# Kernel tuning notes

Hardware: AMD Instinct MI355X
Metric: run time of the kernel (lower is better)

## Reference

```python
import jax, jax.numpy as jnp
import numpy as np


def setup_inputs() -> dict:
    key = jax.random.key(0)
    k1, k2 = jax.random.split(key)
    D, N, M = 256, 1024, 1024
    z_x = jax.random.normal(k1, (1, D, N), dtype=jnp.float32)
    z_y = jax.random.normal(k2, (1, D, M), dtype=jnp.float32)
    return {"z_x": z_x, "z_y": z_y}


def reference(z_x, z_y):
    # squeeze().t(): (1, d, N) -> (N, d)
    x = jnp.squeeze(z_x).T  # (N, d)
    y = jnp.squeeze(z_y).T  # (M, d)
    # L1 compare: s[i, j] = -sum_d |x[i, d] - y[j, d]|  -> (N, M)
    s = -jnp.sum(jnp.abs(x[:, None, :] - y[None, :, :]), axis=-1)
    a = jax.nn.softmax(s, axis=1)  # row-wise softmax
    b = jax.nn.softmax(s, axis=0)  # column-wise softmax
    a = a + b - a * b              # soft union of alignments
    return jnp.sum(a * s) / jnp.sum(a)
```

## Files before the change

kernel.cpp:

```cpp
#include <hip/hip_runtime.h>
#include <math.h>


#define DD 256
#define NN 1024
#define DS 4
#define CH (DD / DS)
#define NQ (NN / 4)

__device__ __forceinline__ float waveMax(float v) {
  #pragma unroll
  for (int off = 32; off; off >>= 1) v = fmaxf(v, __shfl_xor(v, off, 64));
  return v;
}
__device__ __forceinline__ float waveSum(float v) {
  #pragma unroll
  for (int off = 32; off; off >>= 1) v += __shfl_xor(v, off, 64);
  return v;
}
__device__ __forceinline__ float blockMax(float v, float* red) {
  v = waveMax(v);
  __syncthreads();
  if ((threadIdx.x & 63) == 0) red[threadIdx.x >> 6] = v;
  __syncthreads();
  return fmaxf(fmaxf(red[0], red[1]), fmaxf(red[2], red[3]));
}
__device__ __forceinline__ float blockSum(float v, float* red) {
  v = waveSum(v);
  __syncthreads();
  if ((threadIdx.x & 63) == 0) red[threadIdx.x >> 6] = v;
  __syncthreads();
  return red[0] + red[1] + red[2] + red[3];
}


#define SSTEP(YB, dd)                                                          \
  {                                                                            \
    const float* xp_ = xs + (dd) * 32 + g * 8;                                 \
    const float4 xa = *(const float4*)xp_;                                     \
    const float4 xb = *(const float4*)(xp_ + 4);                               \
    acc[0][0] += fabsf(xa.x - YB.x); acc[0][1] += fabsf(xa.x - YB.y);          \
    acc[0][2] += fabsf(xa.x - YB.z); acc[0][3] += fabsf(xa.x - YB.w);          \
    acc[1][0] += fabsf(xa.y - YB.x); acc[1][1] += fabsf(xa.y - YB.y);          \
    acc[1][2] += fabsf(xa.y - YB.z); acc[1][3] += fabsf(xa.y - YB.w);          \
    acc[2][0] += fabsf(xa.z - YB.x); acc[2][1] += fabsf(xa.z - YB.y);          \
    acc[2][2] += fabsf(xa.z - YB.z); acc[2][3] += fabsf(xa.z - YB.w);          \
    acc[3][0] += fabsf(xa.w - YB.x); acc[3][1] += fabsf(xa.w - YB.y);          \
    acc[3][2] += fabsf(xa.w - YB.z); acc[3][3] += fabsf(xa.w - YB.w);          \
    acc[4][0] += fabsf(xb.x - YB.x); acc[4][1] += fabsf(xb.x - YB.y);          \
    acc[4][2] += fabsf(xb.x - YB.z); acc[4][3] += fabsf(xb.x - YB.w);          \
    acc[5][0] += fabsf(xb.y - YB.x); acc[5][1] += fabsf(xb.y - YB.y);          \
    acc[5][2] += fabsf(xb.y - YB.z); acc[5][3] += fabsf(xb.y - YB.w);          \
    acc[6][0] += fabsf(xb.z - YB.x); acc[6][1] += fabsf(xb.z - YB.y);          \
    acc[6][2] += fabsf(xb.z - YB.z); acc[6][3] += fabsf(xb.z - YB.w);          \
    acc[7][0] += fabsf(xb.w - YB.x); acc[7][1] += fabsf(xb.w - YB.y);          \
    acc[7][2] += fabsf(xb.w - YB.z); acc[7][3] += fabsf(xb.w - YB.w);          \
    const int dn_ = ((dd) + 4 < CH) ? (dd) + 4 : CH - 1;                       \
    YB = yp[dn_ * NQ];                                                         \
  }

__global__ __launch_bounds__(256, 2)
void scompute_kernel(const float* __restrict__ zx, const float* __restrict__ zy,
                     float* __restrict__ Sp, float* __restrict__ accum) {
  const int h  = blockIdx.z;
  const int i0 = blockIdx.y * 32;
  const int j0 = blockIdx.x * 256;
  const int t  = threadIdx.x;
  const int g  = t >> 6;
  const int c  = t & 63;
  if (t == 0 && (blockIdx.x | blockIdx.y | blockIdx.z) == 0) {
    accum[0] = 0.f; accum[1] = 0.f; ((unsigned int*)accum)[2] = 0u;
  }

  __shared__ float xs[CH * 32];
  {
    const float4* __restrict__ X4 = (const float4*)zx;
    float4* xs4 = (float4*)xs;
    #pragma unroll
    for (int k = t; k < CH * 8; k += 256) {
      const int dd = k >> 3, rq = k & 7;
      xs4[k] = X4[(h * CH + dd) * NQ + (i0 >> 2) + rq];
    }
  }
  __syncthreads();

  float acc[8][4];
  #pragma unroll
  for (int r = 0; r < 8; ++r)
    #pragma unroll
    for (int q = 0; q < 4; ++q) acc[r][q] = 0.f;

  const float4* __restrict__ yp =
      (const float4*)zy + (size_t)(h * CH) * NQ + (j0 >> 2) + c;
  float4 y0 = yp[0 * NQ];
  float4 y1 = yp[1 * NQ];
  float4 y2 = yp[2 * NQ];
  float4 y3 = yp[3 * NQ];

  #pragma unroll 1
  for (int d = 0; d < CH; d += 4) {
    SSTEP(y0, d + 0)
    SSTEP(y1, d + 1)
    SSTEP(y2, d + 2)
    SSTEP(y3, d + 3)
  }

  float4* __restrict__ S4 = (float4*)Sp + (size_t)h * (NN * NQ);
  #pragma unroll
  for (int r = 0; r < 8; ++r)
    S4[(i0 + g * 8 + r) * NQ + (j0 >> 2) + c] =
        make_float4(acc[r][0], acc[r][1], acc[r][2], acc[r][3]);
}

__global__ __launch_bounds__(256)
void rowcolstats_kernel(float* __restrict__ Sp,
                        float* __restrict__ rmax, float* __restrict__ rsum,
                        float* __restrict__ pm, float* __restrict__ ps) {
  __shared__ float red[4];
  const int t = threadIdx.x;
  const int row0 = blockIdx.x * 4;
  float4* S4 = (float4*)Sp;
  float4 p[4];
  #pragma unroll
  for (int r = 0; r < 4; ++r) {
    float4 v = S4[(row0 + r) * NQ + t];
    #pragma unroll
    for (int hh = 1; hh < DS; ++hh) {
      const float4 q = S4[(size_t)hh * (NN * NQ) + (row0 + r) * NQ + t];
      v.x += q.x; v.y += q.y; v.z += q.z; v.w += q.w;
    }
    S4[(row0 + r) * NQ + t] = v;
    p[r] = v;
  }
  #pragma unroll
  for (int r = 0; r < 4; ++r) {
    float m = fmaxf(fmaxf(-p[r].x, -p[r].y), fmaxf(-p[r].z, -p[r].w));
    m = blockMax(m, red);
    float l = __expf(-p[r].x - m) + __expf(-p[r].y - m) +
              __expf(-p[r].z - m) + __expf(-p[r].w - m);
    l = blockSum(l, red);
    if (t == 0) { rmax[row0 + r] = m; rsum[row0 + r] = l; }
  }
  float4 cm = make_float4(-1e30f, -1e30f, -1e30f, -1e30f);
  #pragma unroll
  for (int r = 0; r < 4; ++r) {
    cm.x = fmaxf(cm.x, -p[r].x); cm.y = fmaxf(cm.y, -p[r].y);
    cm.z = fmaxf(cm.z, -p[r].z); cm.w = fmaxf(cm.w, -p[r].w);
  }
  float4 cl = make_float4(0.f, 0.f, 0.f, 0.f);
  #pragma unroll
  for (int r = 0; r < 4; ++r) {
    cl.x += __expf(-p[r].x - cm.x); cl.y += __expf(-p[r].y - cm.y);
    cl.z += __expf(-p[r].z - cm.z); cl.w += __expf(-p[r].w - cm.w);
  }
  ((float4*)pm)[blockIdx.x * NQ + t] = cm;
  ((float4*)ps)[blockIdx.x * NQ + t] = cl;
}

__global__ __launch_bounds__(256)
void colcombine_kernel(const float* __restrict__ pm, const float* __restrict__ ps,
                       float* __restrict__ cmax, float* __restrict__ csum) {
  __shared__ float sm[4][64], sl[4][64];
  const int t  = threadIdx.x;
  const int jl = t & 63;
  const int pc = t >> 6;
  const int j  = blockIdx.x * 64 + jl;
  float m = -1e30f;
  #pragma unroll 8
  for (int k = 0; k < 64; ++k) m = fmaxf(m, pm[(pc * 64 + k) * NN + j]);
  float l = 0.f;
  #pragma unroll 8
  for (int k = 0; k < 64; ++k)
    l += __expf(pm[(pc * 64 + k) * NN + j] - m) * ps[(pc * 64 + k) * NN + j];
  sm[pc][jl] = m; sl[pc][jl] = l;
  __syncthreads();
  if (pc == 0) {
    float M = fmaxf(fmaxf(sm[0][jl], sm[1][jl]), fmaxf(sm[2][jl], sm[3][jl]));
    float L = sl[0][jl] * __expf(sm[0][jl] - M) + sl[1][jl] * __expf(sm[1][jl] - M) +
              sl[2][jl] * __expf(sm[2][jl] - M) + sl[3][jl] * __expf(sm[3][jl] - M);
    cmax[j] = M; csum[j] = L;
  }
}

__global__ __launch_bounds__(256)
void final_kernel(const float* __restrict__ Sp,
                  const float* __restrict__ rmax, const float* __restrict__ rsum,
                  const float* __restrict__ cmax, const float* __restrict__ csum,
                  float* __restrict__ accum, float* __restrict__ out) {
  __shared__ float redn[4], redd[4];
  const int t = threadIdx.x;
  const int row0 = blockIdx.x * 4;
  const float4* S4 = (const float4*)Sp;
  const float4 cm = ((const float4*)cmax)[t];
  const float4 cs = ((const float4*)csum)[t];
  float un = 0.f, ud = 0.f;
  #pragma unroll
  for (int r = 0; r < 4; ++r) {
    const int row = row0 + r;
    const float rm = rmax[row];
    const float ri = 1.f / rsum[row];
    const float4 p = S4[row * NQ + t];
    {
      const float s = -p.x;
      const float a = __expf(s - rm) * ri;
      const float b = __expf(s - cm.x) / cs.x;
      const float u = a + b - a * b;
      un += u * s; ud += u;
    }
    {
      const float s = -p.y;
      const float a = __expf(s - rm) * ri;
      const float b = __expf(s - cm.y) / cs.y;
      const float u = a + b - a * b;
      un += u * s; ud += u;
    }
    {
      const float s = -p.z;
      const float a = __expf(s - rm) * ri;
      const float b = __expf(s - cm.z) / cs.z;
      const float u = a + b - a * b;
      un += u * s; ud += u;
    }
    {
      const float s = -p.w;
      const float a = __expf(s - rm) * ri;
      const float b = __expf(s - cm.w) / cs.w;
      const float u = a + b - a * b;
      un += u * s; ud += u;
    }
  }
  un = waveSum(un); ud = waveSum(ud);
  if ((t & 63) == 0) { redn[t >> 6] = un; redd[t >> 6] = ud; }
  __syncthreads();
  if (t == 0) {
    atomicAdd(&accum[0], redn[0] + redn[1] + redn[2] + redn[3]);
    atomicAdd(&accum[1], redd[0] + redd[1] + redd[2] + redd[3]);
    __threadfence();
    unsigned int* cnt = (unsigned int*)accum + 2;
    const unsigned int old = atomicAdd(cnt, 1u);
    if (old == gridDim.x - 1) {
      const float n = atomicAdd(&accum[0], 0.f);
      const float d = atomicAdd(&accum[1], 0.f);
      out[0] = n / d;
    }
  }
}


#define TJ  128
#define NCH (NN / TJ)
#define BLK 256

__global__ __launch_bounds__(BLK)
void stats2_kernel(const float* __restrict__ zx, const float* __restrict__ zy,
                   float* __restrict__ partM, float* __restrict__ partS) {
  const int side = blockIdx.z;
  const float* __restrict__ X = side ? zy : zx;
  const float* __restrict__ Y = side ? zx : zy;
  const int j0 = blockIdx.x * TJ;
  const int i0 = blockIdx.y * 8;
  const int t  = threadIdx.x;
  const int rg = t >> 5;
  const int c  = t & 31;

  __shared__ float xs[8 * DD];
  for (int k = t; k < 8 * DD; k += BLK)
    xs[k] = X[(k >> 3) * NN + i0 + (k & 7)];
  __syncthreads();

  const float4* __restrict__ Y4 = (const float4*)Y;
  const int yb = (j0 >> 2) + c;
  float4 acc = make_float4(0.f, 0.f, 0.f, 0.f);
  #pragma unroll 8
  for (int d = 0; d < DD; ++d) {
    const float4 yv = Y4[d * NQ + yb];
    const float xv = xs[d * 8 + rg];
    acc.x += fabsf(xv - yv.x);
    acc.y += fabsf(xv - yv.y);
    acc.z += fabsf(xv - yv.z);
    acc.w += fabsf(xv - yv.w);
  }

  float m = fmaxf(fmaxf(-acc.x, -acc.y), fmaxf(-acc.z, -acc.w));
  #pragma unroll
  for (int off = 16; off > 0; off >>= 1) m = fmaxf(m, __shfl_xor(m, off, 32));
  float p = __expf(-acc.x - m) + __expf(-acc.y - m) +
            __expf(-acc.z - m) + __expf(-acc.w - m);
  #pragma unroll
  for (int off = 16; off > 0; off >>= 1) p += __shfl_xor(p, off, 32);

  if (c == 0) {
    const int idx = side * (NCH * NN) + blockIdx.x * NN + (i0 + rg);
    partM[idx] = m;
    partS[idx] = p;
  }
}

__global__ __launch_bounds__(BLK)
void combine_kernel(const float* __restrict__ partM, const float* __restrict__ partS,
                    float* __restrict__ rmax, float* __restrict__ rsum,
                    float* __restrict__ cmax, float* __restrict__ csum,
                    float* __restrict__ accum) {
  const int gid = blockIdx.x * BLK + threadIdx.x;
  if (gid == 0) { accum[0] = 0.f; accum[1] = 0.f; }
  const int sd = gid >> 10;
  const int i  = gid & (NN - 1);
  float mk[NCH], sk[NCH];
  #pragma unroll
  for (int k = 0; k < NCH; ++k) {
    mk[k] = partM[sd * (NCH * NN) + k * NN + i];
    sk[k] = partS[sd * (NCH * NN) + k * NN + i];
  }
  float m = mk[0];
  #pragma unroll
  for (int k = 1; k < NCH; ++k) m = fmaxf(m, mk[k]);
  float s = 0.f;
  #pragma unroll
  for (int k = 0; k < NCH; ++k) s += __expf(mk[k] - m) * sk[k];
  if (sd == 0) { rmax[i] = m; rsum[i] = s; }
  else         { cmax[i] = m; csum[i] = s; }
}

__global__ __launch_bounds__(BLK)
void final2_kernel(const float* __restrict__ zx, const float* __restrict__ zy,
                   const float* __restrict__ rmax, const float* __restrict__ rsum,
                   const float* __restrict__ cmax, const float* __restrict__ csum,
                   float* __restrict__ accum) {
  const int j0 = blockIdx.x * TJ;
  const int i0 = blockIdx.y * 8;
  const int t  = threadIdx.x;
  const int rg = t >> 5;
  const int c  = t & 31;

  __shared__ float xs[8 * DD];
  __shared__ float redn[4], redd[4];
  for (int k = t; k < 8 * DD; k += BLK)
    xs[k] = zx[(k >> 3) * NN + i0 + (k & 7)];
  __syncthreads();

  const float4* __restrict__ Y4 = (const float4*)zy;
  const int yb = (j0 >> 2) + c;
  float4 acc = make_float4(0.f, 0.f, 0.f, 0.f);
  #pragma unroll 8
  for (int d = 0; d < DD; ++d) {
    const float4 yv = Y4[d * NQ + yb];
    const float xv = xs[d * 8 + rg];
    acc.x += fabsf(xv - yv.x);
    acc.y += fabsf(xv - yv.y);
    acc.z += fabsf(xv - yv.z);
    acc.w += fabsf(xv - yv.w);
  }

  const int i = i0 + rg;
  const float rm = rmax[i];
  const float ri = 1.f / rsum[i];
  const float4 cm = ((const float4*)cmax)[yb];
  const float4 cs = ((const float4*)csum)[yb];

  float un = 0.f, ud = 0.f;
  {
    const float s = -acc.x;
    const float a = __expf(s - rm) * ri;
    const float b = __expf(s - cm.x) / cs.x;
    const float u = a + b - a * b;
    un += u * s; ud += u;
  }
  {
    const float s = -acc.y;
    const float a = __expf(s - rm) * ri;
    const float b = __expf(s - cm.y) / cs.y;
    const float u = a + b - a * b;
    un += u * s; ud += u;
  }
  {
    const float s = -acc.z;
    const float a = __expf(s - rm) * ri;
    const float b = __expf(s - cm.z) / cs.z;
    const float u = a + b - a * b;
    un += u * s; ud += u;
  }
  {
    const float s = -acc.w;
    const float a = __expf(s - rm) * ri;
    const float b = __expf(s - cm.w) / cs.w;
    const float u = a + b - a * b;
    un += u * s; ud += u;
  }

  un = waveSum(un); ud = waveSum(ud);
  if ((t & 63) == 0) { redn[t >> 6] = un; redd[t >> 6] = ud; }
  __syncthreads();
  if (t == 0) {
    atomicAdd(&accum[0], redn[0] + redn[1] + redn[2] + redn[3]);
    atomicAdd(&accum[1], redd[0] + redd[1] + redd[2] + redd[3]);
  }
}

__global__ void finalize_kernel(const float* __restrict__ accum, float* __restrict__ out) {
  out[0] = accum[0] / accum[1];
}


extern "C" void kernel_launch(void* const* d_in, const int* in_sizes, int n_in,
                              void* d_out, int out_size, void* d_ws, size_t ws_size,
                              hipStream_t stream) {
  const float* zx = (const float*)d_in[0];
  const float* zy = (const float*)d_in[1];
  float* ws  = (float*)d_ws;
  float* out = (float*)d_out;

  float* accum = ws;
  float* Sp    = ws + 16;
  float* pm    = Sp + DS * NN * NN;
  float* ps    = pm + 256 * NN;
  float* rmax  = ps + 256 * NN;
  float* rsum  = rmax + NN;
  float* cmax  = rsum + NN;
  float* csum  = cmax + NN;
  const size_t need = (size_t)((csum + NN) - ws) * sizeof(float);

  if (ws_size >= need) {
    dim3 g1(NN / 256, NN / 32, DS);
    scompute_kernel<<<g1, 256, 0, stream>>>(zx, zy, Sp, accum);
    rowcolstats_kernel<<<NN / 4, 256, 0, stream>>>(Sp, rmax, rsum, pm, ps);
    colcombine_kernel<<<NN / 64, 256, 0, stream>>>(pm, ps, cmax, csum);
    final_kernel<<<NN / 4, 256, 0, stream>>>(Sp, rmax, rsum, cmax, csum, accum, out);
  } else {
    float* partM = ws + 16;
    float* partS = partM + 2 * NCH * NN;
    float* frmax = partS + 2 * NCH * NN;
    float* frsum = frmax + NN;
    float* fcmax = frsum + NN;
    float* fcsum = fcmax + NN;
    dim3 sgrid(NCH, NN / 8, 2);
    stats2_kernel<<<sgrid, BLK, 0, stream>>>(zx, zy, partM, partS);
    combine_kernel<<<(2 * NN) / BLK, BLK, 0, stream>>>(partM, partS,
                                                       frmax, frsum, fcmax, fcsum, accum);
    dim3 fgrid(NCH, NN / 8);
    final2_kernel<<<fgrid, BLK, 0, stream>>>(zx, zy, frmax, frsum, fcmax, fcsum, accum);
    finalize_kernel<<<1, 1, 0, stream>>>(accum, out);
  }
}
```

Baseline: 124.5 us.

## Stage Y tiles in double-buffered LDS and halve rows per stats block

The distance kernel now loads Y values into a double-buffered shared-memory tile of eight d-slices per step, prefetching the next tile into registers during compute, instead of streaming them per thread from global memory with a four-deep register pipeline. The row/column stats and final kernels now process two rows per block instead of four, doubling block count to raise parallelism, with the column-partial buffers sized to match. This adds a barrier per tile and extra LDS traffic in exchange for more regular global loads, and doubles the partial column statistics colcombine must reduce.

```diff
diff --git a/kernel.cpp b/kernel.cpp
--- a/kernel.cpp
+++ b/kernel.cpp
@@ -5,8 +5,9 @@
 #define DD 256
 #define NN 1024
 #define DS 4
-#define CH (DD / DS)
-#define NQ (NN / 4)
+#define CH 64
+#define NQ 256
+#define NSTRIPE 512
 
 __device__ __forceinline__ float waveMax(float v) {
   #pragma unroll
@@ -33,55 +34,37 @@
   return red[0] + red[1] + red[2] + red[3];
 }
 
-
-#define SSTEP(YB, dd)                                                          \
-  {                                                                            \
-    const float* xp_ = xs + (dd) * 32 + g * 8;                                 \
-    const float4 xa = *(const float4*)xp_;                                     \
-    const float4 xb = *(const float4*)(xp_ + 4);                               \
-    acc[0][0] += fabsf(xa.x - YB.x); acc[0][1] += fabsf(xa.x - YB.y);          \
-    acc[0][2] += fabsf(xa.x - YB.z); acc[0][3] += fabsf(xa.x - YB.w);          \
-    acc[1][0] += fabsf(xa.y - YB.x); acc[1][1] += fabsf(xa.y - YB.y);          \
-    acc[1][2] += fabsf(xa.y - YB.z); acc[1][3] += fabsf(xa.y - YB.w);          \
-    acc[2][0] += fabsf(xa.z - YB.x); acc[2][1] += fabsf(xa.z - YB.y);          \
-    acc[2][2] += fabsf(xa.z - YB.z); acc[2][3] += fabsf(xa.z - YB.w);          \
-    acc[3][0] += fabsf(xa.w - YB.x); acc[3][1] += fabsf(xa.w - YB.y);          \
-    acc[3][2] += fabsf(xa.w - YB.z); acc[3][3] += fabsf(xa.w - YB.w);          \
-    acc[4][0] += fabsf(xb.x - YB.x); acc[4][1] += fabsf(xb.x - YB.y);          \
-    acc[4][2] += fabsf(xb.x - YB.z); acc[4][3] += fabsf(xb.x - YB.w);          \
-    acc[5][0] += fabsf(xb.y - YB.x); acc[5][1] += fabsf(xb.y - YB.y);          \
-    acc[5][2] += fabsf(xb.y - YB.z); acc[5][3] += fabsf(xb.y - YB.w);          \
-    acc[6][0] += fabsf(xb.z - YB.x); acc[6][1] += fabsf(xb.z - YB.y);          \
-    acc[6][2] += fabsf(xb.z - YB.z); acc[6][3] += fabsf(xb.z - YB.w);          \
-    acc[7][0] += fabsf(xb.w - YB.x); acc[7][1] += fabsf(xb.w - YB.y);          \
-    acc[7][2] += fabsf(xb.w - YB.z); acc[7][3] += fabsf(xb.w - YB.w);          \
-    const int dn_ = ((dd) + 4 < CH) ? (dd) + 4 : CH - 1;                       \
-    YB = yp[dn_ * NQ];                                                         \
-  }
 
 __global__ __launch_bounds__(256, 2)
 void scompute_kernel(const float* __restrict__ zx, const float* __restrict__ zy,
                      float* __restrict__ Sp, float* __restrict__ accum) {
-  const int h  = blockIdx.z;
-  const int i0 = blockIdx.y * 32;
-  const int j0 = blockIdx.x * 256;
-  const int t  = threadIdx.x;
-  const int g  = t >> 6;
-  const int c  = t & 63;
+  const int h   = blockIdx.z;
+  const int i0  = blockIdx.y * 32;
+  const int j0q = blockIdx.x * 64;
+  const int t   = threadIdx.x;
+  const int g   = t >> 6;
+  const int c   = t & 63;
   if (t == 0 && (blockIdx.x | blockIdx.y | blockIdx.z) == 0) {
     accum[0] = 0.f; accum[1] = 0.f; ((unsigned int*)accum)[2] = 0u;
   }
 
-  __shared__ float xs[CH * 32];
+  __shared__ float  xs[CH][32];
+  __shared__ float4 ys[2][8][64];
+
   {
     const float4* __restrict__ X4 = (const float4*)zx;
     float4* xs4 = (float4*)xs;
     #pragma unroll
-    for (int k = t; k < CH * 8; k += 256) {
-      const int dd = k >> 3, rq = k & 7;
-      xs4[k] = X4[(h * CH + dd) * NQ + (i0 >> 2) + rq];
-    }
-  }
+    for (int k = t; k < CH * 8; k += 256)
+      xs4[k] = X4[(h * CH + (k >> 3)) * NQ + (i0 >> 2) + (k & 7)];
+  }
+
+  const float4* __restrict__ Y4 = (const float4*)zy + (size_t)(h * CH) * NQ + j0q;
+  const int sd0 = t >> 6;
+  const int sd1 = 4 + sd0;
+
+  ys[0][sd0][c] = Y4[sd0 * NQ + c];
+  ys[0][sd1][c] = Y4[sd1 * NQ + c];
   __syncthreads();
 
   float acc[8][4];
@@ -90,25 +73,47 @@
     #pragma unroll
     for (int q = 0; q < 4; ++q) acc[r][q] = 0.f;
 
-  const float4* __restrict__ yp =
-      (const float4*)zy + (size_t)(h * CH) * NQ + (j0 >> 2) + c;
-  float4 y0 = yp[0 * NQ];
-  float4 y1 = yp[1 * NQ];
-  float4 y2 = yp[2 * NQ];
-  float4 y3 = yp[3 * NQ];
-
-  #pragma unroll 1
-  for (int d = 0; d < CH; d += 4) {
-    SSTEP(y0, d + 0)
-    SSTEP(y1, d + 1)
-    SSTEP(y2, d + 2)
-    SSTEP(y3, d + 3)
+  for (int n = 0; n < CH / 8; ++n) {
+    const int buf = n & 1;
+    float4 p0, p1;
+    if (n < CH / 8 - 1) {
+      p0 = Y4[(8 * (n + 1) + sd0) * NQ + c];
+      p1 = Y4[(8 * (n + 1) + sd1) * NQ + c];
+    }
+    #pragma unroll
+    for (int dd = 0; dd < 8; ++dd) {
+      const int d = n * 8 + dd;
+      const float4 xa = *(const float4*)&xs[d][g * 8];
+      const float4 xb = *(const float4*)&xs[d][g * 8 + 4];
+      const float4 yv = ys[buf][dd][c];
+      acc[0][0] += fabsf(xa.x - yv.x); acc[0][1] += fabsf(xa.x - yv.y);
+      acc[0][2] += fabsf(xa.x - yv.z); acc[0][3] += fabsf(xa.x - yv.w);
+      acc[1][0] += fabsf(xa.y - yv.x); acc[1][1] += fabsf(xa.y - yv.y);
+      acc[1][2] += fabsf(xa.y - yv.z); acc[1][3] += fabsf(xa.y - yv.w);
+      acc[2][0] += fabsf(xa.z - yv.x); acc[2][1] += fabsf(xa.z - yv.y);
+      acc[2][2] += fabsf(xa.z - yv.z); acc[2][3] += fabsf(xa.z - yv.w);
+      acc[3][0] += fabsf(xa.w - yv.x); acc[3][1] += fabsf(xa.w - yv.y);
+      acc[3][2] += fabsf(xa.w - yv.z); acc[3][3] += fabsf(xa.w - yv.w);
+      acc[4][0] += fabsf(xb.x - yv.x); acc[4][1] += fabsf(xb.x - yv.y);
+      acc[4][2] += fabsf(xb.x - yv.z); acc[4][3] += fabsf(xb.x - yv.w);
+      acc[5][0] += fabsf(xb.y - yv.x); acc[5][1] += fabsf(xb.y - yv.y);
+      acc[5][2] += fabsf(xb.y - yv.z); acc[5][3] += fabsf(xb.y - yv.w);
+      acc[6][0] += fabsf(xb.z - yv.x); acc[6][1] += fabsf(xb.z - yv.y);
+      acc[6][2] += fabsf(xb.z - yv.z); acc[6][3] += fabsf(xb.z - yv.w);
+      acc[7][0] += fabsf(xb.w - yv.x); acc[7][1] += fabsf(xb.w - yv.y);
+      acc[7][2] += fabsf(xb.w - yv.z); acc[7][3] += fabsf(xb.w - yv.w);
+    }
+    if (n < CH / 8 - 1) {
+      ys[buf ^ 1][sd0][c] = p0;
+      ys[buf ^ 1][sd1][c] = p1;
+    }
+    __syncthreads();
   }
 
   float4* __restrict__ S4 = (float4*)Sp + (size_t)h * (NN * NQ);
   #pragma unroll
   for (int r = 0; r < 8; ++r)
-    S4[(i0 + g * 8 + r) * NQ + (j0 >> 2) + c] =
+    S4[(i0 + g * 8 + r) * NQ + j0q + c] =
         make_float4(acc[r][0], acc[r][1], acc[r][2], acc[r][3]);
 }
 
@@ -118,11 +123,11 @@
                         float* __restrict__ pm, float* __restrict__ ps) {
   __shared__ float red[4];
   const int t = threadIdx.x;
-  const int row0 = blockIdx.x * 4;
+  const int row0 = blockIdx.x * 2;
   float4* S4 = (float4*)Sp;
-  float4 p[4];
-  #pragma unroll
-  for (int r = 0; r < 4; ++r) {
+  float4 p[2];
+  #pragma unroll
+  for (int r = 0; r < 2; ++r) {
     float4 v = S4[(row0 + r) * NQ + t];
     #pragma unroll
     for (int hh = 1; hh < DS; ++hh) {
@@ -133,7 +138,7 @@
     p[r] = v;
   }
   #pragma unroll
-  for (int r = 0; r < 4; ++r) {
+  for (int r = 0; r < 2; ++r) {
     float m = fmaxf(fmaxf(-p[r].x, -p[r].y), fmaxf(-p[r].z, -p[r].w));
     m = blockMax(m, red);
     float l = __expf(-p[r].x - m) + __expf(-p[r].y - m) +
@@ -143,13 +148,13 @@
   }
   float4 cm = make_float4(-1e30f, -1e30f, -1e30f, -1e30f);
   #pragma unroll
-  for (int r = 0; r < 4; ++r) {
+  for (int r = 0; r < 2; ++r) {
     cm.x = fmaxf(cm.x, -p[r].x); cm.y = fmaxf(cm.y, -p[r].y);
     cm.z = fmaxf(cm.z, -p[r].z); cm.w = fmaxf(cm.w, -p[r].w);
   }
   float4 cl = make_float4(0.f, 0.f, 0.f, 0.f);
   #pragma unroll
-  for (int r = 0; r < 4; ++r) {
+  for (int r = 0; r < 2; ++r) {
     cl.x += __expf(-p[r].x - cm.x); cl.y += __expf(-p[r].y - cm.y);
     cl.z += __expf(-p[r].z - cm.z); cl.w += __expf(-p[r].w - cm.w);
   }
@@ -167,11 +172,13 @@
   const int j  = blockIdx.x * 64 + jl;
   float m = -1e30f;
   #pragma unroll 8
-  for (int k = 0; k < 64; ++k) m = fmaxf(m, pm[(pc * 64 + k) * NN + j]);
+  for (int k = 0; k < NSTRIPE / 4; ++k)
+    m = fmaxf(m, pm[(pc * (NSTRIPE / 4) + k) * NN + j]);
   float l = 0.f;
   #pragma unroll 8
-  for (int k = 0; k < 64; ++k)
-    l += __expf(pm[(pc * 64 + k) * NN + j] - m) * ps[(pc * 64 + k) * NN + j];
+  for (int k = 0; k < NSTRIPE / 4; ++k)
+    l += __expf(pm[(pc * (NSTRIPE / 4) + k) * NN + j] - m) *
+         ps[(pc * (NSTRIPE / 4) + k) * NN + j];
   sm[pc][jl] = m; sl[pc][jl] = l;
   __syncthreads();
   if (pc == 0) {
@@ -189,13 +196,13 @@
                   float* __restrict__ accum, float* __restrict__ out) {
   __shared__ float redn[4], redd[4];
   const int t = threadIdx.x;
-  const int row0 = blockIdx.x * 4;
+  const int row0 = blockIdx.x * 2;
   const float4* S4 = (const float4*)Sp;
   const float4 cm = ((const float4*)cmax)[t];
   const float4 cs = ((const float4*)csum)[t];
   float un = 0.f, ud = 0.f;
   #pragma unroll
-  for (int r = 0; r < 4; ++r) {
+  for (int r = 0; r < 2; ++r) {
     const int row = row0 + r;
     const float rm = rmax[row];
     const float ri = 1.f / rsum[row];
@@ -412,8 +419,8 @@
   float* accum = ws;
   float* Sp    = ws + 16;
   float* pm    = Sp + DS * NN * NN;
-  float* ps    = pm + 256 * NN;
-  float* rmax  = ps + 256 * NN;
+  float* ps    = pm + NSTRIPE * NN;
+  float* rmax  = ps + NSTRIPE * NN;
   float* rsum  = rmax + NN;
   float* cmax  = rsum + NN;
   float* csum  = cmax + NN;
@@ -422,9 +429,9 @@
   if (ws_size >= need) {
     dim3 g1(NN / 256, NN / 32, DS);
     scompute_kernel<<<g1, 256, 0, stream>>>(zx, zy, Sp, accum);
-    rowcolstats_kernel<<<NN / 4, 256, 0, stream>>>(Sp, rmax, rsum, pm, ps);
+    rowcolstats_kernel<<<NSTRIPE, 256, 0, stream>>>(Sp, rmax, rsum, pm, ps);
     colcombine_kernel<<<NN / 64, 256, 0, stream>>>(pm, ps, cmax, csum);
-    final_kernel<<<NN / 4, 256, 0, stream>>>(Sp, rmax, rsum, cmax, csum, accum, out);
+    final_kernel<<<NN / 2, 256, 0, stream>>>(Sp, rmax, rsum, cmax, csum, accum, out);
   } else {
     float* partM = ws + 16;
     float* partS = partM + 2 * NCH * NN;
```

After: 138.3 us. 1.11x slower.
